# Optimization experiments

Hardware: AMD Instinct MI355X
Metric: run time of the kernel (lower is better)

The kernel has to match this reference:

```python
import jax, jax.numpy as jnp
import numpy as np

N, E, DIN, H, C = 50000, 800000, 128, 2, 64  # C = hidden_dim*heads (per-head out channels); concat=False -> mean over heads -> layer out dim C
NUM_CLASSES = 4
EPS_GN = 1e-5


def setup_inputs() -> dict:
    key = jax.random.key(0)

    def rn(i, shape, scale):
        return (jax.random.normal(jax.random.fold_in(key, i), shape) * scale).astype(jnp.float32)

    inp = {
        "x": rn(0, (N, DIN), 1.0),
        "edge_index": jax.random.randint(jax.random.fold_in(key, 1), (2, E), 0, N, dtype=jnp.int32),
    }
    layer_in = [DIN, C]
    for li, din in enumerate(layer_in, 1):
        s = 1.0 / np.sqrt(din)
        base = 10 * li
        inp[f"Wl{li}"] = rn(base + 0, (din, H * C), s)
        inp[f"bl{li}"] = jnp.zeros((H * C,), jnp.float32)
        inp[f"Wr{li}"] = rn(base + 1, (din, H * C), s)
        inp[f"br{li}"] = jnp.zeros((H * C,), jnp.float32)
        inp[f"att{li}"] = rn(base + 2, (H, C), 1.0 / np.sqrt(C))
        inp[f"bias{li}"] = jnp.zeros((C,), jnp.float32)
        inp[f"gng{li}"] = jnp.ones((C,), jnp.float32)   # GraphNorm weight
        inp[f"gnb{li}"] = jnp.zeros((C,), jnp.float32)  # GraphNorm bias
        inp[f"gna{li}"] = jnp.ones((C,), jnp.float32)   # GraphNorm mean_scale
    inp["W1"] = rn(100, (C, NUM_CLASSES), 1.0 / np.sqrt(C))
    inp["b1"] = jnp.zeros((NUM_CLASSES,), jnp.float32)
    return inp


def gatv2_layer(x, src, dst, Wl, bl, Wr, br, att, bias):
    # PyG GATv2Conv, concat=False. x: [N, din]
    n = x.shape[0]
    xl = (x @ Wl + bl).reshape(n, H, C)  # source transform
    xr = (x @ Wr + br).reshape(n, H, C)  # target transform
    m = jax.nn.leaky_relu(xl[src] + xr[dst], negative_slope=0.2)  # [E', H, C]
    e = jnp.einsum('ehc,hc->eh', m, att)                           # [E', H]
    emax = jax.lax.stop_gradient(jax.ops.segment_max(e, dst, num_segments=n))
    ee = jnp.exp(e - emax[dst])
    denom = jax.ops.segment_sum(ee, dst, num_segments=n)
    alpha = ee / (denom[dst] + 1e-16)                              # softmax over in-edges of each target
    out = jax.ops.segment_sum(alpha[:, :, None] * xl[src], dst, num_segments=n)  # [N, H, C]
    return out.mean(axis=1) + bias  # concat=False -> mean over heads


def graph_norm(x, gamma, beta, mean_scale):
    # single-graph GraphNorm: stats over all nodes, per feature
    mean = x.mean(axis=0, keepdims=True)
    xc = x - mean_scale * mean
    var = (xc * xc).mean(axis=0, keepdims=True)
    return gamma * xc * jax.lax.rsqrt(var + EPS_GN) + beta


def reference(x, edge_index,
              Wl1, bl1, Wr1, br1, att1, bias1, gng1, gnb1, gna1,
              Wl2, bl2, Wr2, br2, att2, bias2, gng2, gnb2, gna2,
              W1, b1):
    src, dst = edge_index[0], edge_index[1]
    loops = jnp.arange(N, dtype=src.dtype)  # add_self_loops=True
    src = jnp.concatenate([src, loops])
    dst = jnp.concatenate([dst, loops])

    h = gatv2_layer(x, src, dst, Wl1, bl1, Wr1, br1, att1, bias1)
    h = graph_norm(h, gng1, gnb1, gna1)
    h = gatv2_layer(h, src, dst, Wl2, bl2, Wr2, br2, att2, bias2)
    h = graph_norm(h, gng2, gnb2, gna2)

    logits = h @ W1 + b1  # dropout is identity in eval
    return jax.nn.log_softmax(logits, axis=1)
```

## Files before the change

kernel.cpp:

```cpp
#include <hip/hip_runtime.h>
#include <hip/hip_bf16.h>
#include <math.h>

#define HC   128
#define CCH  64
#define NBK  256

typedef __attribute__((ext_vector_type(8))) short short8;
typedef __attribute__((ext_vector_type(4))) float floatx4;

__device__ __forceinline__ unsigned short f2bf(float f) {
  unsigned u = __float_as_uint(f);
  u += 0x7fffu + ((u >> 16) & 1u);
  return (unsigned short)(u >> 16);
}

__device__ __forceinline__ void unpack8(uint4 u, float* f) {
  f[0] = __uint_as_float(u.x << 16);
  f[1] = __uint_as_float(u.x & 0xffff0000u);
  f[2] = __uint_as_float(u.y << 16);
  f[3] = __uint_as_float(u.y & 0xffff0000u);
  f[4] = __uint_as_float(u.z << 16);
  f[5] = __uint_as_float(u.z & 0xffff0000u);
  f[6] = __uint_as_float(u.w << 16);
  f[7] = __uint_as_float(u.w & 0xffff0000u);
}

__global__ __launch_bounds__(256) void bin_cast(
    const int* __restrict__ ei, int E, int chunk, int nB,
    int* __restrict__ blkCnt, int* __restrict__ bucketTotal,
    const float* __restrict__ x, unsigned short* __restrict__ xb, int cnt4,
    const float* __restrict__ Wl, const float* __restrict__ Wr,
    unsigned short* __restrict__ Wlt, unsigned short* __restrict__ Wrt) {
  if ((int)blockIdx.x < NBK) {
    __shared__ int cnt[512];
    for (int j = threadIdx.x; j < nB; j += 256) cnt[j] = 0;
    __syncthreads();
    int e0 = blockIdx.x * chunk;
    int e1 = e0 + chunk; e1 = e1 < E ? e1 : E;
    int e = e0 + threadIdx.x;
    for (; e + 768 < e1; e += 1024) {
      int d0 = __builtin_nontemporal_load(ei + E + e);
      int d1 = __builtin_nontemporal_load(ei + E + e + 256);
      int d2 = __builtin_nontemporal_load(ei + E + e + 512);
      int d3 = __builtin_nontemporal_load(ei + E + e + 768);
      atomicAdd(&cnt[d0 >> 7], 1);
      atomicAdd(&cnt[d1 >> 7], 1);
      atomicAdd(&cnt[d2 >> 7], 1);
      atomicAdd(&cnt[d3 >> 7], 1);
    }
    for (; e < e1; e += 256) {
      int dst = __builtin_nontemporal_load(ei + E + e);
      atomicAdd(&cnt[dst >> 7], 1);
    }
    __syncthreads();
    for (int j = threadIdx.x; j < nB; j += 256) {
      int c = cnt[j];
      blkCnt[blockIdx.x * nB + j] = c;
      if (c) atomicAdd(&bucketTotal[j], c);
    }
  } else {
    int gid = (blockIdx.x - NBK) * 256 + threadIdx.x;
    if (gid < 32768) {
      int sel = gid >> 14;
      int i = gid & 16383;
      int nn = i >> 7, k = i & 127;
      const float* W = sel ? Wr : Wl;
      unsigned short* Wt = sel ? Wrt : Wlt;
      Wt[i] = f2bf(W[k * HC + nn]);
    }
    if (gid >= cnt4) return;
    float4 v = ((const float4*)x)[gid];
    ushort4 o;
    o.x = f2bf(v.x); o.y = f2bf(v.y); o.z = f2bf(v.z); o.w = f2bf(v.w);
    ((ushort4*)xb)[gid] = o;
  }
}

__global__ __launch_bounds__(256) void scan_offsets(
    const int* __restrict__ bucketTotal, int* __restrict__ bucketBase,
    int* __restrict__ blkCnt, int nB, int E) {
  const int j = blockIdx.x;
  const int tid = threadIdx.x;
  __shared__ int red[256];
  __shared__ int col[NBK];
  int s = 0;
  for (int k = tid; k < j; k += 256) s += bucketTotal[k];
  red[tid] = s;
  __syncthreads();
  for (int off = 128; off > 0; off >>= 1) {
    if (tid < off) red[tid] += red[tid + off];
    __syncthreads();
  }
  const int base_j = red[0];
  if (tid == 0) {
    bucketBase[j] = base_j;
    if (j == 0) bucketBase[nB] = E;
  }
  int v = 0;
  if (tid < NBK) { v = blkCnt[tid * nB + j]; col[tid] = v; }
  __syncthreads();
  for (int off = 1; off < NBK; off <<= 1) {
    int t = 0;
    if (tid < NBK && tid >= off) t = col[tid - off];
    __syncthreads();
    if (tid < NBK) col[tid] += t;
    __syncthreads();
  }
  if (tid < NBK) blkCnt[tid * nB + j] = base_j + col[tid] - v;
}

__global__ __launch_bounds__(256) void place_gemm1(
    const int* __restrict__ ei, int E, int chunk, int nB,
    const int* __restrict__ blkCnt, unsigned* __restrict__ ebuf,
    const unsigned short* __restrict__ A,
    const unsigned short* __restrict__ Wlt, const unsigned short* __restrict__ Wrt,
    const float* __restrict__ bl, const float* __restrict__ br,
    unsigned short* __restrict__ xlb, unsigned short* __restrict__ xrb, int M) {
  if ((int)blockIdx.x < NBK) {
    __shared__ int cur[512];
    for (int j = threadIdx.x; j < nB; j += 256)
      cur[j] = blkCnt[blockIdx.x * nB + j];
    __syncthreads();
    int e0 = blockIdx.x * chunk;
    int e1 = e0 + chunk; e1 = e1 < E ? e1 : E;
    int e = e0 + threadIdx.x;
    for (; e + 768 < e1; e += 1024) {
      int d0 = __builtin_nontemporal_load(ei + E + e);
      int d1 = __builtin_nontemporal_load(ei + E + e + 256);
      int d2 = __builtin_nontemporal_load(ei + E + e + 512);
      int d3 = __builtin_nontemporal_load(ei + E + e + 768);
      int s0 = __builtin_nontemporal_load(ei + e);
      int s1 = __builtin_nontemporal_load(ei + e + 256);
      int s2 = __builtin_nontemporal_load(ei + e + 512);
      int s3 = __builtin_nontemporal_load(ei + e + 768);
      int p0 = atomicAdd(&cur[d0 >> 7], 1);
      int p1 = atomicAdd(&cur[d1 >> 7], 1);
      int p2 = atomicAdd(&cur[d2 >> 7], 1);
      int p3 = atomicAdd(&cur[d3 >> 7], 1);
      ebuf[p0] = (unsigned)s0 | ((unsigned)(d0 & 127) << 16);
      ebuf[p1] = (unsigned)s1 | ((unsigned)(d1 & 127) << 16);
      ebuf[p2] = (unsigned)s2 | ((unsigned)(d2 & 127) << 16);
      ebuf[p3] = (unsigned)s3 | ((unsigned)(d3 & 127) << 16);
    }
    for (; e < e1; e += 256) {
      int dst = __builtin_nontemporal_load(ei + E + e);
      int src = __builtin_nontemporal_load(ei + e);
      int pos = atomicAdd(&cur[dst >> 7], 1);
      ebuf[pos] = (unsigned)src | ((unsigned)(dst & 127) << 16);
    }
  } else {
    constexpr int K = 128;
    const int w = threadIdx.x >> 6;
    const int lane = threadIdx.x & 63;
    const int row0 = (blockIdx.x - NBK) * 16;
    if (row0 >= M) return;
    const bool isR = w >= 2;
    const unsigned short* Wt = isR ? Wrt : Wlt;
    const float* bias = isR ? br : bl;
    unsigned short* out = isR ? xrb : xlb;
    const int col0 = (w & 1) * 64;
    const int mrow = lane & 15, quad = lane >> 4;
    const unsigned short* pa = A + (size_t)(row0 + mrow) * K + quad * 8;
    const unsigned short* pb = Wt + (size_t)(col0 + mrow) * K + quad * 8;
    floatx4 acc0 = {0.f, 0.f, 0.f, 0.f}, acc1 = acc0, acc2 = acc0, acc3 = acc0;
#pragma unroll
    for (int k0 = 0; k0 < K; k0 += 32) {
      short8 af = *(const short8*)(pa + k0);
      short8 b0 = *(const short8*)(pb + k0);
      short8 b1 = *(const short8*)(pb + 16 * K + k0);
      short8 b2 = *(const short8*)(pb + 32 * K + k0);
      short8 b3 = *(const short8*)(pb + 48 * K + k0);
      acc0 = __builtin_amdgcn_mfma_f32_16x16x32_bf16(af, b0, acc0, 0, 0, 0);
      acc1 = __builtin_amdgcn_mfma_f32_16x16x32_bf16(af, b1, acc1, 0, 0, 0);
      acc2 = __builtin_amdgcn_mfma_f32_16x16x32_bf16(af, b2, acc2, 0, 0, 0);
      acc3 = __builtin_amdgcn_mfma_f32_16x16x32_bf16(af, b3, acc3, 0, 0, 0);
    }
    floatx4 accs[4] = {acc0, acc1, acc2, acc3};
#pragma unroll
    for (int ct = 0; ct < 4; ct++) {
      int col = col0 + ct * 16 + mrow;
      float bv = bias[col];
#pragma unroll
      for (int r = 0; r < 4; r++) {
        int row = row0 + quad * 4 + r;
        if (row < M) out[(size_t)row * HC + col] = f2bf(accs[ct][r] + bv);
      }
    }
  }
}

__global__ __launch_bounds__(256) void csr_build(
    const unsigned* __restrict__ ebuf, const int* __restrict__ bucketBase,
    int* __restrict__ row_start, int* __restrict__ deg,
    int* __restrict__ csr_src, int N, int EPtot) {
  const int b = blockIdx.x;
  const int tid = threadIdx.x;
  const int node0 = b * 128;
  const int nb = (N - node0) < 128 ? (N - node0) : 128;
  const int ebase = bucketBase[b];
  const int eend = bucketBase[b + 1];
  __shared__ int degL[128], scanL[128], curL[128];
  if (tid < 128) degL[tid] = 0;
  __syncthreads();
  for (int e = ebase + tid; e < eend; e += 256)
    atomicAdd(&degL[(ebuf[e] >> 16) & 127], 1);
  __syncthreads();
  if (tid < 128) scanL[tid] = degL[tid];
  __syncthreads();
  for (int off = 1; off < 128; off <<= 1) {
    int t = 0;
    if (tid < 128 && tid >= off) t = scanL[tid - off];
    __syncthreads();
    if (tid < 128) scanL[tid] += t;
    __syncthreads();
  }
  if (tid < 128) {
    int rs = ebase + (scanL[tid] - degL[tid]) + node0 + tid;
    curL[tid] = rs;
    if (tid < nb) {
      row_start[node0 + tid] = rs;
      deg[node0 + tid] = degL[tid];
    }
  }
  __syncthreads();
  for (int e = ebase + tid; e < eend; e += 256) {
    unsigned p = ebuf[e];
    int pos = atomicAdd(&curL[(p >> 16) & 127], 1);
    csr_src[pos] = (int)(p & 0xffffu);
  }
  __syncthreads();
  if (tid < nb) csr_src[curL[tid]] = node0 + tid;
  if (b == 0 && tid < 32) csr_src[EPtot + tid] = 0;
}

template <int K>
__global__ __launch_bounds__(256) void gemm_mfma(
    const unsigned short* __restrict__ A,
    const unsigned short* __restrict__ Wlt, const unsigned short* __restrict__ Wrt,
    const float* __restrict__ bl, const float* __restrict__ br,
    unsigned short* __restrict__ xlb, unsigned short* __restrict__ xrb, int M) {
  const int w = threadIdx.x >> 6;
  const int lane = threadIdx.x & 63;
  const int row0 = blockIdx.x * 16;
  if (row0 >= M) return;
  const bool isR = w >= 2;
  const unsigned short* Wt = isR ? Wrt : Wlt;
  const float* bias = isR ? br : bl;
  unsigned short* out = isR ? xrb : xlb;
  const int col0 = (w & 1) * 64;
  const int mrow = lane & 15, quad = lane >> 4;
  const unsigned short* pa = A + (size_t)(row0 + mrow) * K + quad * 8;
  const unsigned short* pb = Wt + (size_t)(col0 + mrow) * K + quad * 8;
  floatx4 acc0 = {0.f, 0.f, 0.f, 0.f}, acc1 = acc0, acc2 = acc0, acc3 = acc0;
#pragma unroll
  for (int k0 = 0; k0 < K; k0 += 32) {
    short8 af = *(const short8*)(pa + k0);
    short8 b0 = *(const short8*)(pb + k0);
    short8 b1 = *(const short8*)(pb + 16 * K + k0);
    short8 b2 = *(const short8*)(pb + 32 * K + k0);
    short8 b3 = *(const short8*)(pb + 48 * K + k0);
    acc0 = __builtin_amdgcn_mfma_f32_16x16x32_bf16(af, b0, acc0, 0, 0, 0);
    acc1 = __builtin_amdgcn_mfma_f32_16x16x32_bf16(af, b1, acc1, 0, 0, 0);
    acc2 = __builtin_amdgcn_mfma_f32_16x16x32_bf16(af, b2, acc2, 0, 0, 0);
    acc3 = __builtin_amdgcn_mfma_f32_16x16x32_bf16(af, b3, acc3, 0, 0, 0);
  }
  floatx4 accs[4] = {acc0, acc1, acc2, acc3};
#pragma unroll
  for (int ct = 0; ct < 4; ct++) {
    int col = col0 + ct * 16 + mrow;
    float bv = bias[col];
#pragma unroll
    for (int r = 0; r < 4; r++) {
      int row = row0 + quad * 4 + r;
      if (row < M) out[(size_t)row * HC + col] = f2bf(accs[ct][r] + bv);
    }
  }
}

__global__ __launch_bounds__(256) void node_attn(
    const unsigned short* __restrict__ xlb, const unsigned short* __restrict__ xrb,
    const int* __restrict__ csr_src, const int* __restrict__ row_start,
    const int* __restrict__ deg, const float* __restrict__ att,
    const float* __restrict__ bias, unsigned short* __restrict__ outb, int n) {
  int wave = (blockIdx.x * blockDim.x + threadIdx.x) >> 6;
  if (wave >= n) return;
  const int node = wave;
  const int lane = threadIdx.x & 63;
  const int g = lane >> 4;
  const int hl = lane & 15;
  const int c8 = hl << 3;

  float r[8], a[8];
  {
    uint4 u = *(const uint4*)(xrb + (size_t)node * HC + c8);
    unpack8(u, r);
    float4 a0 = *(const float4*)(att + c8);
    float4 a1 = *(const float4*)(att + c8 + 4);
    a[0] = a0.x; a[1] = a0.y; a[2] = a0.z; a[3] = a0.w;
    a[4] = a1.x; a[5] = a1.y; a[6] = a1.z; a[7] = a1.w;
  }

  const int p0 = row_start[node];
  const int pend = p0 + deg[node] + 1;

  float d = 0.f;
  float acc[8] = {0.f, 0.f, 0.f, 0.f, 0.f, 0.f, 0.f, 0.f};

  int s0 = __builtin_nontemporal_load(csr_src + p0 + g);
  uint4 A0 = *(const uint4*)(xlb + (size_t)s0 * HC + c8);
  int s1 = __builtin_nontemporal_load(csr_src + p0 + 4 + g);
  uint4 A1 = *(const uint4*)(xlb + (size_t)s1 * HC + c8);

  for (int p = p0; p < pend; p += 4) {
    int s2 = __builtin_nontemporal_load(csr_src + p + 8 + g);
    uint4 A2 = *(const uint4*)(xlb + (size_t)s2 * HC + c8);

    float v[8];
    unpack8(A0, v);
    float e1 = 0.f, e2 = 0.f;
#pragma unroll
    for (int i = 0; i < 8; i++) {
      float s = v[i] + r[i];
      e1 = fmaf(a[i], s, e1);
      e2 = fmaf(a[i], fabsf(s), e2);
    }
    float e = fmaf(0.4f, e2, 0.6f * e1);
    e += __shfl_xor(e, 1);
    e += __shfl_xor(e, 2);
    e += __shfl_xor(e, 4);

    bool valid = (p + g) < pend;
    float w = valid ? __expf(e) : 0.f;
    d += w;
#pragma unroll
    for (int i = 0; i < 8; i++) acc[i] = fmaf(w, v[i], acc[i]);
    A0 = A1; A1 = A2;
  }

#pragma unroll
  for (int ofs = 16; ofs <= 32; ofs <<= 1) {
    d += __shfl_xor(d, ofs);
#pragma unroll
    for (int i = 0; i < 8; i++) acc[i] += __shfl_xor(acc[i], ofs);
  }
  float inv = 1.f / (d + 1e-16f);
  const float* bb = bias + (c8 & 63);
  float o[8];
#pragma unroll
  for (int i = 0; i < 8; i++) {
    float t = acc[i] * inv;
    float t2 = __shfl_xor(t, 8);
    o[i] = 0.5f * (t + t2) + bb[i];
  }
  if (lane < 8) {
    uint4 ou;
    ou.x = (unsigned)f2bf(o[0]) | ((unsigned)f2bf(o[1]) << 16);
    ou.y = (unsigned)f2bf(o[2]) | ((unsigned)f2bf(o[3]) << 16);
    ou.z = (unsigned)f2bf(o[4]) | ((unsigned)f2bf(o[5]) << 16);
    ou.w = (unsigned)f2bf(o[6]) | ((unsigned)f2bf(o[7]) << 16);
    *(uint4*)(outb + (size_t)node * CCH + c8) = ou;
  }
}

__global__ __launch_bounds__(256) void gn_stats(
    const unsigned short* __restrict__ y, float* __restrict__ S, int n) {
  __shared__ float l1a[256], l1b[256], l2a[256], l2b[256];
  int half = threadIdx.x & 31;
  int sub = threadIdx.x >> 5;
  float s1a = 0.f, s1b = 0.f, s2a = 0.f, s2b = 0.f;
  int stride = gridDim.x * 8;
  for (int r = blockIdx.x * 8 + sub; r < n; r += stride) {
    unsigned u = ((const unsigned*)(y + (size_t)r * CCH))[half];
    float va = __uint_as_float(u << 16);
    float vb = __uint_as_float(u & 0xffff0000u);
    s1a += va; s2a = fmaf(va, va, s2a);
    s1b += vb; s2b = fmaf(vb, vb, s2b);
  }
  l1a[threadIdx.x] = s1a; l1b[threadIdx.x] = s1b;
  l2a[threadIdx.x] = s2a; l2b[threadIdx.x] = s2b;
  __syncthreads();
  if (threadIdx.x < 32) {
#pragma unroll
    for (int k = 1; k < 8; k++) {
      s1a += l1a[threadIdx.x + 32 * k];
      s1b += l1b[threadIdx.x + 32 * k];
      s2a += l2a[threadIdx.x + 32 * k];
      s2b += l2b[threadIdx.x + 32 * k];
    }
    atomicAdd(&S[2 * half], s1a);
    atomicAdd(&S[2 * half + 1], s1b);
    atomicAdd(&S[64 + 2 * half], s2a);
    atomicAdd(&S[64 + 2 * half + 1], s2b);
  }
}

__global__ __launch_bounds__(256) void gn_stats_prep(
    const unsigned short* __restrict__ y, float* __restrict__ S,
    int* __restrict__ done, const float* __restrict__ gamma,
    const float* __restrict__ beta, const float* __restrict__ mscale,
    const float* __restrict__ Wl2, const float* __restrict__ bl2,
    const float* __restrict__ Wr2, const float* __restrict__ br2,
    unsigned short* __restrict__ Wl2tb, float* __restrict__ bl2p,
    unsigned short* __restrict__ Wr2tb, float* __restrict__ br2p, int n) {
  __shared__ float l1a[256], l1b[256], l2a[256], l2b[256];
  int half = threadIdx.x & 31;
  int sub = threadIdx.x >> 5;
  float s1a = 0.f, s1b = 0.f, s2a = 0.f, s2b = 0.f;
  int stride = gridDim.x * 8;
  for (int r = blockIdx.x * 8 + sub; r < n; r += stride) {
    unsigned u = ((const unsigned*)(y + (size_t)r * CCH))[half];
    float va = __uint_as_float(u << 16);
    float vb = __uint_as_float(u & 0xffff0000u);
    s1a += va; s2a = fmaf(va, va, s2a);
    s1b += vb; s2b = fmaf(vb, vb, s2b);
  }
  l1a[threadIdx.x] = s1a; l1b[threadIdx.x] = s1b;
  l2a[threadIdx.x] = s2a; l2b[threadIdx.x] = s2b;
  __syncthreads();
  if (threadIdx.x < 32) {
#pragma unroll
    for (int k = 1; k < 8; k++) {
      s1a += l1a[threadIdx.x + 32 * k];
      s1b += l1b[threadIdx.x + 32 * k];
      s2a += l2a[threadIdx.x + 32 * k];
      s2b += l2b[threadIdx.x + 32 * k];
    }
    atomicAdd(&S[2 * half], s1a);
    atomicAdd(&S[2 * half + 1], s1b);
    atomicAdd(&S[64 + 2 * half], s2a);
    atomicAdd(&S[64 + 2 * half + 1], s2b);
  }
  __threadfence();
  __shared__ int isLast;
  if (threadIdx.x == 0) {
    int old = atomicAdd(done, 1);
    isLast = (old == (int)gridDim.x - 1) ? 1 : 0;
  }
  __syncthreads();
  if (!isLast) return;
  __threadfence();
  __shared__ float As[64], Bs[64];
  int t = threadIdx.x;
  if (t < 64) {
    float invn = 1.f / (float)n;
    float mu = S[t] * invn;
    float ms = mscale[t];
    float var = S[64 + t] * invn - 2.f * ms * mu * mu + ms * ms * mu * mu;
    float A = gamma[t] * rsqrtf(var + 1e-5f);
    As[t] = A;
    Bs[t] = beta[t] - A * ms * mu;
  }
  __syncthreads();
  const int side = t >> 7, col = t & 127;
  const float* W = side ? Wr2 : Wl2;
  unsigned short* Wt = side ? Wr2tb : Wl2tb;
  const float* bin = side ? br2 : bl2;
  float* bout = side ? br2p : bl2p;
  float s = 0.f;
  for (int c = 0; c < 64; c++) {
    float w = W[c * HC + col];
    Wt[col * 64 + c] = f2bf(As[c] * w);
    s = fmaf(Bs[c], w, s);
  }
  bout[col] = bin[col] + s;
}

__global__ __launch_bounds__(256) void classify(
    const unsigned short* __restrict__ h,
    const float* __restrict__ S, const float* __restrict__ gamma,
    const float* __restrict__ beta, const float* __restrict__ mscale,
    const float* __restrict__ W, const float* __restrict__ b,
    float* __restrict__ out, int n) {
  __shared__ float4 sW[64];
  __shared__ float sBt[256];
  __shared__ float sb[4];
  int tid = threadIdx.x;
  if (tid < 64) {
    float invn = 1.f / (float)n;
    float mu = S[tid] * invn;
    float ms = mscale[tid];
    float var = S[64 + tid] * invn - 2.f * ms * mu * mu + ms * ms * mu * mu;
    float A = gamma[tid] * rsqrtf(var + 1e-5f);
    float B = beta[tid] - A * ms * mu;
    float4 w = ((const float4*)W)[tid];
    sW[tid] = make_float4(A * w.x, A * w.y, A * w.z, A * w.w);
    sBt[tid * 4 + 0] = B * w.x; sBt[tid * 4 + 1] = B * w.y;
    sBt[tid * 4 + 2] = B * w.z; sBt[tid * 4 + 3] = B * w.w;
  }
  __syncthreads();
  if (tid < 4) {
    float s = b[tid];
    for (int c = 0; c < 64; c++) s += sBt[c * 4 + tid];
    sb[tid] = s;
  }
  __syncthreads();
  int node = blockIdx.x * 256 + tid;
  if (node >= n) return;
  float acc0 = sb[0], acc1 = sb[1], acc2 = sb[2], acc3 = sb[3];
  const uint4* row = (const uint4*)(h + (size_t)node * CCH);
#pragma unroll
  for (int k4 = 0; k4 < 8; k4++) {
    uint4 u = row[k4];
    float v[8];
    unpack8(u, v);
#pragma unroll
    for (int j = 0; j < 8; j++) {
      float4 w = sW[k4 * 8 + j];
      acc0 = fmaf(v[j], w.x, acc0);
      acc1 = fmaf(v[j], w.y, acc1);
      acc2 = fmaf(v[j], w.z, acc2);
      acc3 = fmaf(v[j], w.w, acc3);
    }
  }
  float mx = fmaxf(fmaxf(acc0, acc1), fmaxf(acc2, acc3));
  float s = __expf(acc0 - mx) + __expf(acc1 - mx) + __expf(acc2 - mx) + __expf(acc3 - mx);
  float lse = mx + logf(s);
  float4 o = make_float4(acc0 - lse, acc1 - lse, acc2 - lse, acc3 - lse);
  *((float4*)(out + (size_t)node * 4)) = o;
}

extern "C" void kernel_launch(void* const* d_in, const int* in_sizes, int n_in,
                              void* d_out, int out_size, void* d_ws, size_t ws_size,
                              hipStream_t stream) {
  const float* x     = (const float*)d_in[0];
  const int*   ei    = (const int*)d_in[1];
  const float* Wl1   = (const float*)d_in[2];
  const float* bl1   = (const float*)d_in[3];
  const float* Wr1   = (const float*)d_in[4];
  const float* br1   = (const float*)d_in[5];
  const float* att1  = (const float*)d_in[6];
  const float* bias1 = (const float*)d_in[7];
  const float* gng1  = (const float*)d_in[8];
  const float* gnb1  = (const float*)d_in[9];
  const float* gna1  = (const float*)d_in[10];
  const float* Wl2   = (const float*)d_in[11];
  const float* bl2   = (const float*)d_in[12];
  const float* Wr2   = (const float*)d_in[13];
  const float* br2   = (const float*)d_in[14];
  const float* att2  = (const float*)d_in[15];
  const float* bias2 = (const float*)d_in[16];
  const float* gng2  = (const float*)d_in[17];
  const float* gnb2  = (const float*)d_in[18];
  const float* gna2  = (const float*)d_in[19];
  const float* W1    = (const float*)d_in[20];
  const float* b1    = (const float*)d_in[21];

  const int N = in_sizes[0] / 128;
  const int E = in_sizes[1] / 2;
  const int EP = E + N;
  const int nB = (N + 127) >> 7;
  const int chunk = (E + NBK - 1) / NBK;

  int* bucketTotal = (int*)d_ws;
  float* S1  = (float*)(bucketTotal + 512);
  float* S2  = S1 + 128;
  int* done  = (int*)(S2 + 128);
  float* bl2p = (float*)(done + 64);
  float* br2p = bl2p + 128;
  unsigned short* xb    = (unsigned short*)(br2p + 128);
  unsigned short* xlb   = xb + (size_t)N * HC;
  unsigned short* xrb   = xlb + (size_t)N * HC;
  unsigned short* aggb  = xrb + (size_t)N * HC;
  unsigned short* Wl1tb = aggb + (size_t)N * CCH;
  unsigned short* Wr1tb = Wl1tb + HC * HC;
  unsigned short* Wl2tb = Wr1tb + HC * HC;
  unsigned short* Wr2tb = Wl2tb + HC * CCH;
  int* bucketBase = (int*)(Wr2tb + HC * CCH);
  int* blkCnt  = bucketBase + 512 + 8;
  int* row_st  = blkCnt + NBK * 512;
  int* deg     = row_st + N;
  unsigned* ebuf = (unsigned*)(deg + N);
  int* csr_src = (int*)(ebuf + E);

  dim3 b256(256);
  const int gNode = (N * 64 + 255) / 256;
  const int gCls  = (N + 255) / 256;
  const int gCast = (N * 32 + 255) / 256;
  const int gGemm = (N + 15) / 16;

  hipMemsetAsync(d_ws, 0, 4096, stream);

  bin_cast<<<NBK + gCast, b256, 0, stream>>>(
      ei, E, chunk, nB, blkCnt, bucketTotal,
      x, xb, N * 32, Wl1, Wr1, Wl1tb, Wr1tb);

  scan_offsets<<<nB, b256, 0, stream>>>(bucketTotal, bucketBase, blkCnt, nB, E);

  place_gemm1<<<NBK + gGemm, b256, 0, stream>>>(
      ei, E, chunk, nB, blkCnt, ebuf,
      xb, Wl1tb, Wr1tb, bl1, br1, xlb, xrb, N);

  csr_build<<<nB, b256, 0, stream>>>(ebuf, bucketBase, row_st, deg, csr_src, N, EP);

  node_attn<<<gNode, b256, 0, stream>>>(xlb, xrb, csr_src, row_st, deg, att1, bias1, aggb, N);
  gn_stats_prep<<<256, b256, 0, stream>>>(aggb, S1, done, gng1, gnb1, gna1,
                                          Wl2, bl2, Wr2, br2,
                                          Wl2tb, bl2p, Wr2tb, br2p, N);

  gemm_mfma<64><<<gGemm, b256, 0, stream>>>(aggb, Wl2tb, Wr2tb, bl2p, br2p, xlb, xrb, N);
  node_attn<<<gNode, b256, 0, stream>>>(xlb, xrb, csr_src, row_st, deg, att2, bias2, aggb, N);
  gn_stats<<<256, b256, 0, stream>>>(aggb, S2, N);

  classify<<<gCls, b256, 0, stream>>>(aggb, S2, gng2, gnb2, gna2, W1, b1,
                                      (float*)d_out, N);
}
```

Measured before the change: 339.2 us.

## Process 32 rows per GEMM block, deepen gather prefetch, use exp2 in attention

The GEMM blocks now compute two 16-row tiles per wave, so each loaded weight fragment feeds two MFMAs and the grid is halved. The attention kernel prefetches one more neighbour group (three in flight instead of two) to hide gather latency. It also folds log2(e) into the attention vector so it can call exp2f instead of __expf. The cost is more registers per thread, which may reduce occupancy, and slightly different rounding in the softmax weights.

```diff
diff --git a/kernel.cpp b/kernel.cpp
--- a/kernel.cpp
+++ b/kernel.cpp
@@ -24,6 +24,61 @@
   f[5] = __uint_as_float(u.z & 0xffff0000u);
   f[6] = __uint_as_float(u.w << 16);
   f[7] = __uint_as_float(u.w & 0xffff0000u);
+}
+
+template <int K>
+__device__ __forceinline__ void gemm32rows(
+    const unsigned short* __restrict__ A,
+    const unsigned short* __restrict__ Wlt, const unsigned short* __restrict__ Wrt,
+    const float* __restrict__ bl, const float* __restrict__ br,
+    unsigned short* __restrict__ xlb, unsigned short* __restrict__ xrb,
+    int M, int row0, int tid) {
+  const int w = tid >> 6;
+  const int lane = tid & 63;
+  const bool isR = w >= 2;
+  const unsigned short* Wt = isR ? Wrt : Wlt;
+  const float* bias = isR ? br : bl;
+  unsigned short* out = isR ? xrb : xlb;
+  const int col0 = (w & 1) * 64;
+  const int mrow = lane & 15, quad = lane >> 4;
+  const unsigned short* pa0 = A + (size_t)(row0 + mrow) * K + quad * 8;
+  const unsigned short* pa1 = pa0 + (size_t)16 * K;
+  const unsigned short* pb = Wt + (size_t)(col0 + mrow) * K + quad * 8;
+  floatx4 acc[2][4];
+#pragma unroll
+  for (int gp = 0; gp < 2; gp++)
+#pragma unroll
+    for (int ct = 0; ct < 4; ct++) acc[gp][ct] = (floatx4){0.f, 0.f, 0.f, 0.f};
+#pragma unroll
+  for (int k0 = 0; k0 < K; k0 += 32) {
+    short8 a0 = *(const short8*)(pa0 + k0);
+    short8 a1 = *(const short8*)(pa1 + k0);
+    short8 b0 = *(const short8*)(pb + k0);
+    short8 b1 = *(const short8*)(pb + 16 * K + k0);
+    short8 b2 = *(const short8*)(pb + 32 * K + k0);
+    short8 b3 = *(const short8*)(pb + 48 * K + k0);
+    acc[0][0] = __builtin_amdgcn_mfma_f32_16x16x32_bf16(a0, b0, acc[0][0], 0, 0, 0);
+    acc[1][0] = __builtin_amdgcn_mfma_f32_16x16x32_bf16(a1, b0, acc[1][0], 0, 0, 0);
+    acc[0][1] = __builtin_amdgcn_mfma_f32_16x16x32_bf16(a0, b1, acc[0][1], 0, 0, 0);
+    acc[1][1] = __builtin_amdgcn_mfma_f32_16x16x32_bf16(a1, b1, acc[1][1], 0, 0, 0);
+    acc[0][2] = __builtin_amdgcn_mfma_f32_16x16x32_bf16(a0, b2, acc[0][2], 0, 0, 0);
+    acc[1][2] = __builtin_amdgcn_mfma_f32_16x16x32_bf16(a1, b2, acc[1][2], 0, 0, 0);
+    acc[0][3] = __builtin_amdgcn_mfma_f32_16x16x32_bf16(a0, b3, acc[0][3], 0, 0, 0);
+    acc[1][3] = __builtin_amdgcn_mfma_f32_16x16x32_bf16(a1, b3, acc[1][3], 0, 0, 0);
+  }
+#pragma unroll
+  for (int gp = 0; gp < 2; gp++) {
+#pragma unroll
+    for (int ct = 0; ct < 4; ct++) {
+      int col = col0 + ct * 16 + mrow;
+      float bv = bias[col];
+#pragma unroll
+      for (int r = 0; r < 4; r++) {
+        int row = row0 + gp * 16 + quad * 4 + r;
+        if (row < M) out[(size_t)row * HC + col] = f2bf(acc[gp][ct][r] + bv);
+      }
+    }
+  }
 }
 
 __global__ __launch_bounds__(256) void bin_cast(
@@ -150,43 +205,9 @@
       ebuf[pos] = (unsigned)src | ((unsigned)(dst & 127) << 16);
     }
   } else {
-    constexpr int K = 128;
-    const int w = threadIdx.x >> 6;
-    const int lane = threadIdx.x & 63;
-    const int row0 = (blockIdx.x - NBK) * 16;
+    const int row0 = (blockIdx.x - NBK) * 32;
     if (row0 >= M) return;
-    const bool isR = w >= 2;
-    const unsigned short* Wt = isR ? Wrt : Wlt;
-    const float* bias = isR ? br : bl;
-    unsigned short* out = isR ? xrb : xlb;
-    const int col0 = (w & 1) * 64;
-    const int mrow = lane & 15, quad = lane >> 4;
-    const unsigned short* pa = A + (size_t)(row0 + mrow) * K + quad * 8;
-    const unsigned short* pb = Wt + (size_t)(col0 + mrow) * K + quad * 8;
-    floatx4 acc0 = {0.f, 0.f, 0.f, 0.f}, acc1 = acc0, acc2 = acc0, acc3 = acc0;
-#pragma unroll
-    for (int k0 = 0; k0 < K; k0 += 32) {
-      short8 af = *(const short8*)(pa + k0);
-      short8 b0 = *(const short8*)(pb + k0);
-      short8 b1 = *(const short8*)(pb + 16 * K + k0);
-      short8 b2 = *(const short8*)(pb + 32 * K + k0);
-      short8 b3 = *(const short8*)(pb + 48 * K + k0);
-      acc0 = __builtin_amdgcn_mfma_f32_16x16x32_bf16(af, b0, acc0, 0, 0, 0);
-      acc1 = __builtin_amdgcn_mfma_f32_16x16x32_bf16(af, b1, acc1, 0, 0, 0);
-      acc2 = __builtin_amdgcn_mfma_f32_16x16x32_bf16(af, b2, acc2, 0, 0, 0);
-      acc3 = __builtin_amdgcn_mfma_f32_16x16x32_bf16(af, b3, acc3, 0, 0, 0);
-    }
-    floatx4 accs[4] = {acc0, acc1, acc2, acc3};
-#pragma unroll
-    for (int ct = 0; ct < 4; ct++) {
-      int col = col0 + ct * 16 + mrow;
-      float bv = bias[col];
-#pragma unroll
-      for (int r = 0; r < 4; r++) {
-        int row = row0 + quad * 4 + r;
-        if (row < M) out[(size_t)row * HC + col] = f2bf(accs[ct][r] + bv);
-      }
-    }
+    gemm32rows<128>(A, Wlt, Wrt, bl, br, xlb, xrb, M, row0, threadIdx.x);
   }
 }
 
@@ -240,42 +261,9 @@
     const unsigned short* __restrict__ Wlt, const unsigned short* __restrict__ Wrt,
     const float* __restrict__ bl, const float* __restrict__ br,
     unsigned short* __restrict__ xlb, unsigned short* __restrict__ xrb, int M) {
-  const int w = threadIdx.x >> 6;
-  const int lane = threadIdx.x & 63;
-  const int row0 = blockIdx.x * 16;
+  const int row0 = blockIdx.x * 32;
   if (row0 >= M) return;
-  const bool isR = w >= 2;
-  const unsigned short* Wt = isR ? Wrt : Wlt;
-  const float* bias = isR ? br : bl;
-  unsigned short* out = isR ? xrb : xlb;
-  const int col0 = (w & 1) * 64;
-  const int mrow = lane & 15, quad = lane >> 4;
-  const unsigned short* pa = A + (size_t)(row0 + mrow) * K + quad * 8;
-  const unsigned short* pb = Wt + (size_t)(col0 + mrow) * K + quad * 8;
-  floatx4 acc0 = {0.f, 0.f, 0.f, 0.f}, acc1 = acc0, acc2 = acc0, acc3 = acc0;
-#pragma unroll
-  for (int k0 = 0; k0 < K; k0 += 32) {
-    short8 af = *(const short8*)(pa + k0);
-    short8 b0 = *(const short8*)(pb + k0);
-    short8 b1 = *(const short8*)(pb + 16 * K + k0);
-    short8 b2 = *(const short8*)(pb + 32 * K + k0);
-    short8 b3 = *(const short8*)(pb + 48 * K + k0);
-    acc0 = __builtin_amdgcn_mfma_f32_16x16x32_bf16(af, b0, acc0, 0, 0, 0);
-    acc1 = __builtin_amdgcn_mfma_f32_16x16x32_bf16(af, b1, acc1, 0, 0, 0);
-    acc2 = __builtin_amdgcn_mfma_f32_16x16x32_bf16(af, b2, acc2, 0, 0, 0);
-    acc3 = __builtin_amdgcn_mfma_f32_16x16x32_bf16(af, b3, acc3, 0, 0, 0);
-  }
-  floatx4 accs[4] = {acc0, acc1, acc2, acc3};
-#pragma unroll
-  for (int ct = 0; ct < 4; ct++) {
-    int col = col0 + ct * 16 + mrow;
-    float bv = bias[col];
-#pragma unroll
-    for (int r = 0; r < 4; r++) {
-      int row = row0 + quad * 4 + r;
-      if (row < M) out[(size_t)row * HC + col] = f2bf(accs[ct][r] + bv);
-    }
-  }
+  gemm32rows<K>(A, Wlt, Wrt, bl, br, xlb, xrb, M, row0, threadIdx.x);
 }
 
 __global__ __launch_bounds__(256) void node_attn(
@@ -297,8 +285,9 @@
     unpack8(u, r);
     float4 a0 = *(const float4*)(att + c8);
     float4 a1 = *(const float4*)(att + c8 + 4);
-    a[0] = a0.x; a[1] = a0.y; a[2] = a0.z; a[3] = a0.w;
-    a[4] = a1.x; a[5] = a1.y; a[6] = a1.z; a[7] = a1.w;
+    const float L2E = 1.44269504f;
+    a[0] = a0.x * L2E; a[1] = a0.y * L2E; a[2] = a0.z * L2E; a[3] = a0.w * L2E;
+    a[4] = a1.x * L2E; a[5] = a1.y * L2E; a[6] = a1.z * L2E; a[7] = a1.w * L2E;
   }
 
   const int p0 = row_start[node];
@@ -311,10 +300,12 @@
   uint4 A0 = *(const uint4*)(xlb + (size_t)s0 * HC + c8);
   int s1 = __builtin_nontemporal_load(csr_src + p0 + 4 + g);
   uint4 A1 = *(const uint4*)(xlb + (size_t)s1 * HC + c8);
+  int s2 = __builtin_nontemporal_load(csr_src + p0 + 8 + g);
+  uint4 A2 = *(const uint4*)(xlb + (size_t)s2 * HC + c8);
 
   for (int p = p0; p < pend; p += 4) {
-    int s2 = __builtin_nontemporal_load(csr_src + p + 8 + g);
-    uint4 A2 = *(const uint4*)(xlb + (size_t)s2 * HC + c8);
+    int s3 = __builtin_nontemporal_load(csr_src + p + 12 + g);
+    uint4 A3 = *(const uint4*)(xlb + (size_t)s3 * HC + c8);
 
     float v[8];
     unpack8(A0, v);
@@ -331,11 +322,11 @@
     e += __shfl_xor(e, 4);
 
     bool valid = (p + g) < pend;
-    float w = valid ? __expf(e) : 0.f;
+    float w = valid ? exp2f(e) : 0.f;
     d += w;
 #pragma unroll
     for (int i = 0; i < 8; i++) acc[i] = fmaf(w, v[i], acc[i]);
-    A0 = A1; A1 = A2;
+    A0 = A1; A1 = A2; A2 = A3;
   }
 
 #pragma unroll
@@ -577,7 +568,7 @@
   const int gNode = (N * 64 + 255) / 256;
   const int gCls  = (N + 255) / 256;
   const int gCast = (N * 32 + 255) / 256;
-  const int gGemm = (N + 15) / 16;
+  const int gGemm = (N + 31) / 32;
 
   hipMemsetAsync(d_ws, 0, 4096, stream);
 
```

New measurement: 331.6 us. 1.02x faster.
